# Kernel tuning notes

Measured on AMD Instinct MI355X. Metric: run time of the kernel, lower is better.

## Reference

```python
import jax, jax.numpy as jnp
import numpy as np

N_NODES = 50000


def gcn_conv(x, src, dst, W, b):
    # PyG GCNConv: h = D^-1/2 (A+I) D^-1/2 (x W) + b, aggregation at dst.
    n = x.shape[0]
    deg = jax.ops.segment_sum(jnp.ones_like(dst, dtype=x.dtype), dst, num_segments=n)
    dinv = jnp.where(deg > 0, jax.lax.rsqrt(deg), 0.0)
    norm = dinv[src] * dinv[dst]                      # [E]
    h = x @ W                                         # [N, out]
    msg = h[src] * norm[:, None]                      # [E, out] gather
    out = jax.ops.segment_sum(msg, dst, num_segments=n)  # scatter-add
    return out + b


def setup_inputs() -> dict:
    key = jax.random.key(0)
    k1, k2, k3, k4 = jax.random.split(key, 4)
    in_dim, hid, out_dim = 128, 256, 128
    x = jax.random.normal(k1, (N_NODES, in_dim), dtype=jnp.float32)
    edge_index = jax.random.randint(k2, (2, 800000), 0, N_NODES, dtype=jnp.int64)
    s1 = 1.0 / np.sqrt(in_dim)
    s2 = 1.0 / np.sqrt(hid)
    W1 = jax.random.uniform(k3, (in_dim, hid), jnp.float32, -s1, s1)
    b1 = jnp.zeros((hid,), jnp.float32)
    W2 = jax.random.uniform(k4, (hid, out_dim), jnp.float32, -s2, s2)
    b2 = jnp.zeros((out_dim,), jnp.float32)
    return {"x": x, "edge_index": edge_index, "W1": W1, "b1": b1, "W2": W2, "b2": b2}


def reference(x, edge_index, W1, b1, W2, b2):
    n = x.shape[0]
    loops = jnp.arange(n, dtype=edge_index.dtype)
    src = jnp.concatenate([edge_index[0], loops])  # add self-loops
    dst = jnp.concatenate([edge_index[1], loops])
    h = jax.nn.relu(gcn_conv(x, src, dst, W1, b1))
    # dropout in eval mode -> identity
    return gcn_conv(h, src, dst, W2, b2)
```

## Files before the change

### kernel.cpp

```cpp
#include <hip/hip_runtime.h>
#include <hip/hip_bf16.h>


typedef __bf16 bf16x8v __attribute__((ext_vector_type(8)));
typedef short  s16x8   __attribute__((ext_vector_type(8)));
typedef float  f32x4   __attribute__((ext_vector_type(4)));

#define IN_DIM 128
#define HID    256
#define OUTD   128
#define BKT_SHIFT 7
#define BKT_NODES 128
#define MAXB 512
#define CAP  8192
#define EBLK 512

__device__ __forceinline__ float2 bf2f(__hip_bfloat162 v) {
    return make_float2(__bfloat162float(v.x), __bfloat162float(v.y));
}
__device__ __forceinline__ __hip_bfloat162 f2bf(float a, float b) {
    __hip_bfloat162 r; r.x = __float2bfloat16(a); r.y = __float2bfloat16(b); return r;
}
__device__ __forceinline__ void acc_row(float* acc, s16x8 r) {
    __hip_bfloat162* p = (__hip_bfloat162*)&r;
#pragma unroll
    for (int j = 0; j < 4; ++j) {
        float2 f = bf2f(p[j]);
        acc[2 * j]     += f.x;
        acc[2 * j + 1] += f.y;
    }
}

__device__ __forceinline__ int detect_f32(const void* W2raw) {
    const unsigned short* u = (const unsigned short*)W2raw;
    int f32 = 0;
#pragma unroll
    for (int i = 0; i < 64; ++i) {
        unsigned e = (u[i] >> 7) & 0xFF;
        if (e >= 0x7F) f32 = 1;
    }
    return f32;
}
__device__ __forceinline__ int detect_i64(const void* eiraw) {
    const unsigned* ip = (const unsigned*)eiraw;
    unsigned orodd = 0;
#pragma unroll
    for (int i = 0; i < 64; ++i) orodd |= ip[2 * i + 1];
    return (orodd == 0) ? 1 : 0;
}

__device__ __forceinline__ short ldw(const void* raw, int idx, int f32) {
    if (f32) {
        __hip_bfloat16 h = __float2bfloat16(((const float*)raw)[idx]);
        return *(short*)&h;
    }
    return ((const short*)raw)[idx];
}

template <int K, int NN>
__device__ __forceinline__ void swz_one(const void* Wraw, int f32,
                                        short* __restrict__ Bsw, int tid) {
    constexpr int KC = K / 32;
    constexpr int NT = NN / 16;
    if (tid >= NT * KC * 64) return;
    int lane = tid & 63;
    int kc   = (tid >> 6) % KC;
    int nt   = tid / (64 * KC);
    int n  = nt * 16 + (lane & 15);
    int kb = kc * 32 + (lane >> 4) * 8;
    s16x8 v;
#pragma unroll
    for (int j = 0; j < 8; ++j) v[j] = ldw(Wraw, (kb + j) * NN + n, f32);
    ((s16x8*)Bsw)[tid] = v;
}


__global__ __launch_bounds__(256) void k_pe(
        const void* __restrict__ ei_, int E, int N, int NB,
        int* __restrict__ bcnt, unsigned* __restrict__ ppack,
        const void* W1raw, const void* b1raw, const void* W2raw, const void* b2raw,
        short* __restrict__ Bsw1, short* __restrict__ Bsw2,
        __hip_bfloat16* __restrict__ b1c, __hip_bfloat16* __restrict__ b2c,
        int* __restrict__ flags) {
    int blk = blockIdx.x, t = threadIdx.x;
    if (blk >= EBLK) {
        int f32 = detect_f32(W2raw);
        int pb = blk - EBLK;
        if (pb < 16) {
            swz_one<IN_DIM, HID>(W1raw, f32, Bsw1, pb * 256 + t);
        } else if (pb < 32) {
            swz_one<HID, OUTD>(W2raw, f32, Bsw2, (pb - 16) * 256 + t);
        } else {
            short s1 = ldw(b1raw, t, f32);
            b1c[t] = *(__hip_bfloat16*)&s1;
            if (t < OUTD) {
                short s2 = ldw(b2raw, t, f32);
                b2c[t] = *(__hip_bfloat16*)&s2;
            }
            if (t == 0) {
                flags[0] = f32;
                flags[1] = detect_i64(ei_);
            }
        }
        return;
    }
    __shared__ int lhist[4][MAXB];
    __shared__ int lbase[4][MAXB];
    int wv = t >> 6;
    int i64 = detect_i64(ei_);
    const long long* p64 = (const long long*)ei_;
    const int*       p32 = (const int*)ei_;
    int per = (E + EBLK - 1) / EBLK;
    int e0 = blk * per, e1 = min(e0 + per, E);
    for (int i = t; i < NB; i += 256) {
        lhist[0][i] = 0; lhist[1][i] = 0; lhist[2][i] = 0; lhist[3][i] = 0;
    }
    __syncthreads();
    for (int e = e0 + t; e < e1; e += 256) {
        int d = i64 ? (int)p64[E + e] : p32[E + e];
        if ((unsigned)d >= (unsigned)N) d = 0;
        atomicAdd(&lhist[wv][((unsigned)d) >> BKT_SHIFT], 1);
    }
    __syncthreads();
    for (int i = t; i < NB; i += 256) {
        int c0 = lhist[0][i], c1 = lhist[1][i], c2 = lhist[2][i], c3 = lhist[3][i];
        int tot = c0 + c1 + c2 + c3;
        int g = tot ? atomicAdd(&bcnt[i], tot) : 0;
        lbase[0][i] = g;
        lbase[1][i] = g + c0;
        lbase[2][i] = g + c0 + c1;
        lbase[3][i] = g + c0 + c1 + c2;
        lhist[0][i] = 0; lhist[1][i] = 0; lhist[2][i] = 0; lhist[3][i] = 0;
    }
    __syncthreads();
    for (int e = e0 + t; e < e1; e += 256) {
        int d = i64 ? (int)p64[E + e] : p32[E + e];
        int s = i64 ? (int)p64[e]     : p32[e];
        if ((unsigned)d >= (unsigned)N) d = 0;
        if ((unsigned)s >= (unsigned)N) s = 0;
        int b = ((unsigned)d) >> BKT_SHIFT;
        int pos = lbase[wv][b] + atomicAdd(&lhist[wv][b], 1);
        if (pos < CAP)
            ppack[(size_t)b * CAP + pos] = ((unsigned)(d & (BKT_NODES - 1)) << 25) | (unsigned)s;
    }
}


__global__ __launch_bounds__(512) void k_bsort(const int* __restrict__ bcnt,
                                               const unsigned* __restrict__ ppack,
                                               int NB,
                                               int* __restrict__ csr, int* __restrict__ offsets,
                                               float* __restrict__ dinv, int N,
                                               const void* __restrict__ xraw,
                                               const int* __restrict__ flags,
                                               __hip_bfloat16* __restrict__ xs) {
    __shared__ int sb[MAXB];
    __shared__ int h[BKT_NODES], base[BKT_NODES], s[BKT_NODES];
    __shared__ float sdv[BKT_NODES];
    int b = blockIdx.x;
    int t = threadIdx.x;
    int c = (t < NB) ? min(bcnt[t], CAP) : 0;
    sb[t] = c;
    __syncthreads();
    for (int off = 1; off < MAXB; off <<= 1) {
        int u = (t >= off) ? sb[t - off] : 0;
        __syncthreads();
        sb[t] += u;
        __syncthreads();
    }
    int cnt   = min(bcnt[b], CAP);
    int ebase = sb[b] - cnt;
    if (b == NB - 1 && t == 0) offsets[N] = sb[b];
    const unsigned* pp = ppack + (size_t)b * CAP;
    if (t < BKT_NODES) h[t] = 0;
    __syncthreads();
    for (int e = t; e < cnt; e += 512) atomicAdd(&h[pp[e] >> 25], 1);
    __syncthreads();
    int v = (t < BKT_NODES) ? h[t] : 0;
    if (t < BKT_NODES) s[t] = v;
    __syncthreads();
    for (int off = 1; off < BKT_NODES; off <<= 1) {
        int u = (t < BKT_NODES && t >= off) ? s[t - off] : 0;
        __syncthreads();
        if (t < BKT_NODES) s[t] += u;
        __syncthreads();
    }
    if (t < BKT_NODES) {
        int excl = s[t] - v;
        base[t] = excl;
        int node = b * BKT_NODES + t;
        float dv = 0.f;
        if (node < N) {
            dv = rsqrtf((float)(v + 1));
            offsets[node] = ebase + excl;
            dinv[node] = dv;
        } else {
            dinv[node] = 0.f;
        }
        sdv[t] = dv;
        h[t] = 0;
    }
    __syncthreads();
    for (int e = t; e < cnt; e += 512) {
        unsigned pk = pp[e];
        int ld = pk >> 25;
        int pos = ebase + base[ld] + atomicAdd(&h[ld], 1);
        csr[pos] = (int)(pk & 0x1FFFFFFu);
    }
    int f32 = flags[0];
    if (!f32) {
        const s16x8* xg = (const s16x8*)xraw;
        s16x8* xo = (s16x8*)xs;
        for (int u = t; u < BKT_NODES * 16; u += 512) {
            int row = u >> 4;
            int node = b * BKT_NODES + row;
            float dv = sdv[row];
            s16x8 val = {0, 0, 0, 0, 0, 0, 0, 0};
            if (node < N) {
                s16x8 xin = xg[(size_t)node * 16 + (u & 15)];
                __hip_bfloat162* xp = (__hip_bfloat162*)&xin;
                __hip_bfloat162* vp = (__hip_bfloat162*)&val;
#pragma unroll
                for (int j = 0; j < 4; ++j) {
                    float2 f = bf2f(xp[j]);
                    vp[j] = f2bf(dv * f.x, dv * f.y);
                }
            }
            xo[(size_t)node * 16 + (u & 15)] = val;
        }
    } else {
        const float4* xg = (const float4*)xraw;
        __hip_bfloat162* xo = (__hip_bfloat162*)xs;
        for (int u = t; u < BKT_NODES * 32; u += 512) {
            int row = u >> 5;
            int node = b * BKT_NODES + row;
            float dv = sdv[row];
            __hip_bfloat162 v0 = f2bf(0.f, 0.f), v1 = v0;
            if (node < N) {
                float4 xin = xg[(size_t)node * 32 + (u & 31)];
                v0 = f2bf(dv * xin.x, dv * xin.y);
                v1 = f2bf(dv * xin.z, dv * xin.w);
            }
            xo[(size_t)node * 64 + (u & 31) * 2]     = v0;
            xo[(size_t)node * 64 + (u & 31) * 2 + 1] = v1;
        }
    }
}


__global__ __launch_bounds__(256) void k_agg1(
        const s16x8* __restrict__ xs8, const int* __restrict__ offsets,
        const int* __restrict__ csr, const float* __restrict__ dinv,
        s16x8* __restrict__ a8, int N, int Npad, int nwaves) {
    int gw   = blockIdx.x * 4 + (threadIdx.x >> 6);
    int lane = threadIdx.x & 63;
    int g = lane >> 4, li = lane & 15;
    for (int v = gw; v < Npad; v += nwaves) {
        if (v >= N) {
            if (g == 0) { s16x8 z = {0,0,0,0,0,0,0,0}; a8[(size_t)v * 16 + li] = z; }
            continue;
        }
        float acc[8];
#pragma unroll
        for (int j = 0; j < 8; ++j) acc[j] = 0.f;
        int o0 = offsets[v], o1 = offsets[v + 1];
        if (g == 0) acc_row(acc, xs8[(size_t)v * 16 + li]);
        int e = o0 + g;
        for (; e + 12 < o1; e += 16) {
            int s0 = csr[e], s1 = csr[e + 4], s2 = csr[e + 8], s3 = csr[e + 12];
            s16x8 r0 = xs8[(size_t)s0 * 16 + li];
            s16x8 r1 = xs8[(size_t)s1 * 16 + li];
            s16x8 r2 = xs8[(size_t)s2 * 16 + li];
            s16x8 r3 = xs8[(size_t)s3 * 16 + li];
            acc_row(acc, r0); acc_row(acc, r1); acc_row(acc, r2); acc_row(acc, r3);
        }
        for (; e < o1; e += 4) acc_row(acc, xs8[(size_t)csr[e] * 16 + li]);
#pragma unroll
        for (int j = 0; j < 8; ++j) {
            acc[j] += __shfl_xor(acc[j], 16, 64);
            acc[j] += __shfl_xor(acc[j], 32, 64);
        }
        if (g == 0) {
            float dv = dinv[v];
            s16x8 outv;
            __hip_bfloat162* op = (__hip_bfloat162*)&outv;
#pragma unroll
            for (int j = 0; j < 4; ++j) op[j] = f2bf(dv * acc[2 * j], dv * acc[2 * j + 1]);
            a8[(size_t)v * 16 + li] = outv;
        }
    }
}


__global__ __launch_bounds__(256) void k_gemm12(
        const __hip_bfloat16* __restrict__ A, const __hip_bfloat16* __restrict__ Bsw1,
        const __hip_bfloat16* __restrict__ b1c, const __hip_bfloat16* __restrict__ Bsw2,
        const float* __restrict__ dinv, __hip_bfloat16* __restrict__ h2s) {
    __shared__ __align__(16) __hip_bfloat16 hl[64 * HID];
    int wave = threadIdx.x >> 6, lane = threadIdx.x & 63;
    int quad = lane >> 4, l16 = lane & 15;
    int mw = wave * 16;
    int gm = blockIdx.x * 64 + mw;

    bf16x8v a1f[4];
#pragma unroll
    for (int kc = 0; kc < 4; ++kc)
        a1f[kc] = *reinterpret_cast<const bf16x8v*>(
            A + (size_t)(gm + l16) * IN_DIM + kc * 32 + quad * 8);

    const bf16x8v* B1 = reinterpret_cast<const bf16x8v*>(Bsw1);
    for (int nt = 0; nt < HID / 16; ++nt) {
        f32x4 acc = {0.f, 0.f, 0.f, 0.f};
#pragma unroll
        for (int kc = 0; kc < 4; ++kc)
            acc = __builtin_amdgcn_mfma_f32_16x16x32_bf16(a1f[kc], B1[(nt * 4 + kc) * 64 + lane], acc, 0, 0, 0);
        int col = nt * 16 + l16;
        int gcol = col >> 3, csub = col & 7;
        float bv = __bfloat162float(b1c[col]);
#pragma unroll
        for (int r = 0; r < 4; ++r) {
            float v0 = acc[r] + bv; v0 = v0 > 0.f ? v0 : 0.f;
            int r0 = mw + quad * 4 + r;
            ((__hip_bfloat16*)((char*)hl + (size_t)r0 * (HID * 2) + ((gcol ^ (r0 & 31)) << 4)))[csub] = __float2bfloat16(v0);
        }
    }

    bf16x8v a2f[8];
#pragma unroll
    for (int kc = 0; kc < 8; ++kc) {
        int row = mw + l16;
        int g = (kc * 4 + quad) ^ (row & 31);
        a2f[kc] = *reinterpret_cast<const bf16x8v*>(
            (char*)hl + (size_t)row * (HID * 2) + ((size_t)g << 4));
    }
    const bf16x8v* B2 = reinterpret_cast<const bf16x8v*>(Bsw2);
    int rb0 = gm + quad * 4;
    float sc0[4];
#pragma unroll
    for (int r = 0; r < 4; ++r) sc0[r] = dinv[rb0 + r];
    for (int nt = 0; nt < OUTD / 16; ++nt) {
        f32x4 acc = {0.f, 0.f, 0.f, 0.f};
#pragma unroll
        for (int kc = 0; kc < 8; ++kc)
            acc = __builtin_amdgcn_mfma_f32_16x16x32_bf16(a2f[kc], B2[(nt * 8 + kc) * 64 + lane], acc, 0, 0, 0);
        int col = nt * 16 + l16;
#pragma unroll
        for (int r = 0; r < 4; ++r)
            h2s[(size_t)(rb0 + r) * OUTD + col] = __float2bfloat16(acc[r] * sc0[r]);
    }
}


__global__ __launch_bounds__(256) void k_agg2(
        const s16x8* __restrict__ h8, const int* __restrict__ offsets,
        const int* __restrict__ csr, const float* __restrict__ dinv,
        const __hip_bfloat16* __restrict__ b2c, const int* __restrict__ flags,
        void* __restrict__ outraw, int N, int nwaves) {
    int gw   = blockIdx.x * 4 + (threadIdx.x >> 6);
    int lane = threadIdx.x & 63;
    int g = lane >> 4, li = lane & 15;
    int f32 = flags[0];
    float bb[8];
    {
        s16x8 bv = ((const s16x8*)b2c)[li];
        __hip_bfloat162* bp = (__hip_bfloat162*)&bv;
#pragma unroll
        for (int j = 0; j < 4; ++j) {
            float2 f = bf2f(bp[j]);
            bb[2 * j] = f.x; bb[2 * j + 1] = f.y;
        }
    }
    for (int v = gw; v < N; v += nwaves) {
        float acc[8];
#pragma unroll
        for (int j = 0; j < 8; ++j) acc[j] = 0.f;
        int o0 = offsets[v], o1 = offsets[v + 1];
        if (g == 0) acc_row(acc, h8[(size_t)v * 16 + li]);
        int e = o0 + g;
        for (; e + 12 < o1; e += 16) {
            int s0 = csr[e], s1 = csr[e + 4], s2 = csr[e + 8], s3 = csr[e + 12];
            s16x8 r0 = h8[(size_t)s0 * 16 + li];
            s16x8 r1 = h8[(size_t)s1 * 16 + li];
            s16x8 r2 = h8[(size_t)s2 * 16 + li];
            s16x8 r3 = h8[(size_t)s3 * 16 + li];
            acc_row(acc, r0); acc_row(acc, r1); acc_row(acc, r2); acc_row(acc, r3);
        }
        for (; e < o1; e += 4) acc_row(acc, h8[(size_t)csr[e] * 16 + li]);
#pragma unroll
        for (int j = 0; j < 8; ++j) {
            acc[j] += __shfl_xor(acc[j], 16, 64);
            acc[j] += __shfl_xor(acc[j], 32, 64);
        }
        if (g == 0) {
            float dv = dinv[v];
            if (f32) {
                float4* of = (float4*)outraw;
                float4 o0v = {dv * acc[0] + bb[0], dv * acc[1] + bb[1],
                              dv * acc[2] + bb[2], dv * acc[3] + bb[3]};
                float4 o1v = {dv * acc[4] + bb[4], dv * acc[5] + bb[5],
                              dv * acc[6] + bb[6], dv * acc[7] + bb[7]};
                of[(size_t)v * 32 + li * 2]     = o0v;
                of[(size_t)v * 32 + li * 2 + 1] = o1v;
            } else {
                s16x8 outv;
                __hip_bfloat162* op = (__hip_bfloat162*)&outv;
#pragma unroll
                for (int j = 0; j < 4; ++j)
                    op[j] = f2bf(dv * acc[2 * j] + bb[2 * j], dv * acc[2 * j + 1] + bb[2 * j + 1]);
                ((s16x8*)outraw)[(size_t)v * 16 + li] = outv;
            }
        }
    }
}


extern "C" void kernel_launch(void* const* d_in, const int* in_sizes, int n_in,
                              void* d_out, int out_size, void* d_ws, size_t ws_size,
                              hipStream_t stream) {
    const void* x  = d_in[0];
    const void* ei = d_in[1];
    const void* W1 = d_in[2];
    const void* b1 = d_in[3];
    const void* W2 = d_in[4];
    const void* b2 = d_in[5];

    const int N = in_sizes[0] / IN_DIM;
    const int E = in_sizes[1] / 2;
    const int Npad = ((N + 127) / 128) * 128;
    const int NB = Npad / BKT_NODES;

    char* w = (char*)d_ws;
    auto alloc = [&](size_t bytes) -> void* {
        void* p = (void*)w;
        w += (bytes + 255) / 256 * 256;
        return p;
    };
    int*   flags   = (int*)alloc(256);
    int*   bcnt    = (int*)alloc((size_t)MAXB * 4);
    int*   offsets = (int*)alloc((size_t)(N + 1) * 4);
    float* dinv    = (float*)alloc((size_t)Npad * 4);
    unsigned* ppack = (unsigned*)alloc((size_t)NB * CAP * 4);
    int*   csr     = (int*)alloc((size_t)E * 4);
    short* Bsw1 = (short*)alloc((size_t)IN_DIM * HID * 2);
    short* Bsw2 = (short*)alloc((size_t)HID * OUTD * 2);
    __hip_bfloat16* b1c = (__hip_bfloat16*)alloc((size_t)HID * 2);
    __hip_bfloat16* b2c = (__hip_bfloat16*)alloc((size_t)OUTD * 2);
    __hip_bfloat16* xs  = (__hip_bfloat16*)alloc((size_t)Npad * IN_DIM * 2);
    __hip_bfloat16* a1  = (__hip_bfloat16*)alloc((size_t)Npad * IN_DIM * 2);
    __hip_bfloat16* h2s = xs;

    hipMemsetAsync(bcnt, 0, (size_t)MAXB * 4, stream);

    k_pe<<<EBLK + 33, 256, 0, stream>>>(ei, E, N, NB, bcnt, ppack,
                                        W1, b1, W2, b2, Bsw1, Bsw2, b1c, b2c, flags);

    k_bsort<<<NB, 512, 0, stream>>>(bcnt, ppack, NB, csr, offsets, dinv, N,
                                    x, flags, xs);

    const int aggBlocks = 3072, nwaves = aggBlocks * 4;
    k_agg1<<<aggBlocks, 256, 0, stream>>>((const s16x8*)xs, offsets, csr, dinv,
                                          (s16x8*)a1, N, Npad, nwaves);

    k_gemm12<<<Npad / 64, 256, 0, stream>>>(a1, (const __hip_bfloat16*)Bsw1, b1c,
                                            (const __hip_bfloat16*)Bsw2, dinv, h2s);

    k_agg2<<<aggBlocks, 256, 0, stream>>>((const s16x8*)h2s, offsets, csr, dinv,
                                          b2c, flags, d_out, N, nwaves);
}
```

Before: 213.5 us.

## Split feature columns into chunk-major layout to shrink gather working set

Feature matrices xs, a1 and h2s are stored chunk-major: four 32-column slabs, each contiguous over nodes. The aggregation kernels launch one grid section per slab, and each wave handles one node with 16 edge groups of 4 lanes. The intent is to cut the random-gather working set per slab (about 3.2 MB of bf16) so it stays cache-resident, at the cost of reading the CSR and offsets four times and using smaller 64-byte gathers. The GEMM load and store indexing is updated to the new layout.

Result: slower. 289.8 us (+35.7%).

```diff
diff --git a/kernel.cpp b/kernel.cpp
--- a/kernel.cpp
+++ b/kernel.cpp
@@ -14,6 +14,8 @@
 #define MAXB 512
 #define CAP  8192
 #define EBLK 512
+#define NCHUNK 4
+#define AGG_CBLK 2048
 
 __device__ __forceinline__ float2 bf2f(__hip_bfloat162 v) {
     return make_float2(__bfloat162float(v.x), __bfloat162float(v.y));
@@ -150,7 +152,7 @@
                                                const unsigned* __restrict__ ppack,
                                                int NB,
                                                int* __restrict__ csr, int* __restrict__ offsets,
-                                               float* __restrict__ dinv, int N,
+                                               float* __restrict__ dinv, int N, int Npad,
                                                const void* __restrict__ xraw,
                                                const int* __restrict__ flags,
                                                __hip_bfloat16* __restrict__ xs) {
@@ -213,11 +215,12 @@
         s16x8* xo = (s16x8*)xs;
         for (int u = t; u < BKT_NODES * 16; u += 512) {
             int row = u >> 4;
+            int sl  = u & 15;
             int node = b * BKT_NODES + row;
             float dv = sdv[row];
             s16x8 val = {0, 0, 0, 0, 0, 0, 0, 0};
             if (node < N) {
-                s16x8 xin = xg[(size_t)node * 16 + (u & 15)];
+                s16x8 xin = xg[(size_t)node * 16 + sl];
                 __hip_bfloat162* xp = (__hip_bfloat162*)&xin;
                 __hip_bfloat162* vp = (__hip_bfloat162*)&val;
 #pragma unroll
@@ -226,23 +229,25 @@
                     vp[j] = f2bf(dv * f.x, dv * f.y);
                 }
             }
-            xo[(size_t)node * 16 + (u & 15)] = val;
+            xo[((size_t)(sl >> 2) * Npad + node) * 4 + (sl & 3)] = val;
         }
     } else {
         const float4* xg = (const float4*)xraw;
         __hip_bfloat162* xo = (__hip_bfloat162*)xs;
         for (int u = t; u < BKT_NODES * 32; u += 512) {
             int row = u >> 5;
+            int q   = u & 31;
             int node = b * BKT_NODES + row;
             float dv = sdv[row];
             __hip_bfloat162 v0 = f2bf(0.f, 0.f), v1 = v0;
             if (node < N) {
-                float4 xin = xg[(size_t)node * 32 + (u & 31)];
+                float4 xin = xg[(size_t)node * 32 + q];
                 v0 = f2bf(dv * xin.x, dv * xin.y);
                 v1 = f2bf(dv * xin.z, dv * xin.w);
             }
-            xo[(size_t)node * 64 + (u & 31) * 2]     = v0;
-            xo[(size_t)node * 64 + (u & 31) * 2 + 1] = v1;
+            size_t bi = ((size_t)(q >> 3) * Npad + node) * 16 + (q & 7) * 2;
+            xo[bi]     = v0;
+            xo[bi + 1] = v1;
         }
     }
 }
@@ -252,31 +257,29 @@
         const s16x8* __restrict__ xs8, const int* __restrict__ offsets,
         const int* __restrict__ csr, const float* __restrict__ dinv,
         s16x8* __restrict__ a8, int N, int Npad, int nwaves) {
-    int gw   = blockIdx.x * 4 + (threadIdx.x >> 6);
+    int chunk = blockIdx.x / AGG_CBLK;
+    int cb    = blockIdx.x % AGG_CBLK;
+    int gw   = cb * 4 + (threadIdx.x >> 6);
     int lane = threadIdx.x & 63;
-    int g = lane >> 4, li = lane & 15;
+    int g = lane >> 2, li = lane & 3;
+    const s16x8* xc = xs8 + (size_t)chunk * Npad * 4;
+    s16x8*       ac = a8  + (size_t)chunk * Npad * 4;
     for (int v = gw; v < Npad; v += nwaves) {
         if (v >= N) {
-            if (g == 0) { s16x8 z = {0,0,0,0,0,0,0,0}; a8[(size_t)v * 16 + li] = z; }
+            if (g == 0) { s16x8 z = {0,0,0,0,0,0,0,0}; ac[(size_t)v * 4 + li] = z; }
             continue;
         }
         float acc[8];
 #pragma unroll
         for (int j = 0; j < 8; ++j) acc[j] = 0.f;
         int o0 = offsets[v], o1 = offsets[v + 1];
-        if (g == 0) acc_row(acc, xs8[(size_t)v * 16 + li]);
-        int e = o0 + g;
-        for (; e + 12 < o1; e += 16) {
-            int s0 = csr[e], s1 = csr[e + 4], s2 = csr[e + 8], s3 = csr[e + 12];
-            s16x8 r0 = xs8[(size_t)s0 * 16 + li];
-            s16x8 r1 = xs8[(size_t)s1 * 16 + li];
-            s16x8 r2 = xs8[(size_t)s2 * 16 + li];
-            s16x8 r3 = xs8[(size_t)s3 * 16 + li];
-            acc_row(acc, r0); acc_row(acc, r1); acc_row(acc, r2); acc_row(acc, r3);
-        }
-        for (; e < o1; e += 4) acc_row(acc, xs8[(size_t)csr[e] * 16 + li]);
+        if (g == 0) acc_row(acc, xc[(size_t)v * 4 + li]);
+        for (int e = o0 + g; e < o1; e += 16)
+            acc_row(acc, xc[(size_t)csr[e] * 4 + li]);
 #pragma unroll
         for (int j = 0; j < 8; ++j) {
+            acc[j] += __shfl_xor(acc[j], 4, 64);
+            acc[j] += __shfl_xor(acc[j], 8, 64);
             acc[j] += __shfl_xor(acc[j], 16, 64);
             acc[j] += __shfl_xor(acc[j], 32, 64);
         }
@@ -286,7 +289,7 @@
             __hip_bfloat162* op = (__hip_bfloat162*)&outv;
 #pragma unroll
             for (int j = 0; j < 4; ++j) op[j] = f2bf(dv * acc[2 * j], dv * acc[2 * j + 1]);
-            a8[(size_t)v * 16 + li] = outv;
+            ac[(size_t)v * 4 + li] = outv;
         }
     }
 }
@@ -295,7 +298,7 @@
 __global__ __launch_bounds__(256) void k_gemm12(
         const __hip_bfloat16* __restrict__ A, const __hip_bfloat16* __restrict__ Bsw1,
         const __hip_bfloat16* __restrict__ b1c, const __hip_bfloat16* __restrict__ Bsw2,
-        const float* __restrict__ dinv, __hip_bfloat16* __restrict__ h2s) {
+        const float* __restrict__ dinv, __hip_bfloat16* __restrict__ h2s, int Npad) {
     __shared__ __align__(16) __hip_bfloat16 hl[64 * HID];
     int wave = threadIdx.x >> 6, lane = threadIdx.x & 63;
     int quad = lane >> 4, l16 = lane & 15;
@@ -306,7 +309,7 @@
 #pragma unroll
     for (int kc = 0; kc < 4; ++kc)
         a1f[kc] = *reinterpret_cast<const bf16x8v*>(
-            A + (size_t)(gm + l16) * IN_DIM + kc * 32 + quad * 8);
+            A + ((size_t)kc * Npad + gm + l16) * 32 + quad * 8);
 
     const bf16x8v* B1 = reinterpret_cast<const bf16x8v*>(Bsw1);
     for (int nt = 0; nt < HID / 16; ++nt) {
@@ -346,7 +349,7 @@
         int col = nt * 16 + l16;
 #pragma unroll
         for (int r = 0; r < 4; ++r)
-            h2s[(size_t)(rb0 + r) * OUTD + col] = __float2bfloat16(acc[r] * sc0[r]);
+            h2s[((size_t)(nt >> 1) * Npad + rb0 + r) * 32 + (col & 31)] = __float2bfloat16(acc[r] * sc0[r]);
     }
 }
 
@@ -355,14 +358,17 @@
         const s16x8* __restrict__ h8, const int* __restrict__ offsets,
         const int* __restrict__ csr, const float* __restrict__ dinv,
         const __hip_bfloat16* __restrict__ b2c, const int* __restrict__ flags,
-        void* __restrict__ outraw, int N, int nwaves) {
-    int gw   = blockIdx.x * 4 + (threadIdx.x >> 6);
+        void* __restrict__ outraw, int N, int Npad, int nwaves) {
+    int chunk = blockIdx.x / AGG_CBLK;
+    int cb    = blockIdx.x % AGG_CBLK;
+    int gw   = cb * 4 + (threadIdx.x >> 6);
     int lane = threadIdx.x & 63;
-    int g = lane >> 4, li = lane & 15;
+    int g = lane >> 2, li = lane & 3;
     int f32 = flags[0];
+    const s16x8* hc = h8 + (size_t)chunk * Npad * 4;
     float bb[8];
     {
-        s16x8 bv = ((const s16x8*)b2c)[li];
+        s16x8 bv = ((const s16x8*)b2c)[chunk * 4 + li];
         __hip_bfloat162* bp = (__hip_bfloat162*)&bv;
 #pragma unroll
         for (int j = 0; j < 4; ++j) {
@@ -375,19 +381,13 @@
 #pragma unroll
         for (int j = 0; j < 8; ++j) acc[j] = 0.f;
         int o0 = offsets[v], o1 = offsets[v + 1];
-        if (g == 0) acc_row(acc, h8[(size_t)v * 16 + li]);
-        int e = o0 + g;
-        for (; e + 12 < o1; e += 16) {
-            int s0 = csr[e], s1 = csr[e + 4], s2 = csr[e + 8], s3 = csr[e + 12];
-            s16x8 r0 = h8[(size_t)s0 * 16 + li];
-            s16x8 r1 = h8[(size_t)s1 * 16 + li];
-            s16x8 r2 = h8[(size_t)s2 * 16 + li];
-            s16x8 r3 = h8[(size_t)s3 * 16 + li];
-            acc_row(acc, r0); acc_row(acc, r1); acc_row(acc, r2); acc_row(acc, r3);
-        }
-        for (; e < o1; e += 4) acc_row(acc, h8[(size_t)csr[e] * 16 + li]);
+        if (g == 0) acc_row(acc, hc[(size_t)v * 4 + li]);
+        for (int e = o0 + g; e < o1; e += 16)
+            acc_row(acc, hc[(size_t)csr[e] * 4 + li]);
 #pragma unroll
         for (int j = 0; j < 8; ++j) {
+            acc[j] += __shfl_xor(acc[j], 4, 64);
+            acc[j] += __shfl_xor(acc[j], 8, 64);
             acc[j] += __shfl_xor(acc[j], 16, 64);
             acc[j] += __shfl_xor(acc[j], 32, 64);
         }
@@ -399,15 +399,15 @@
                               dv * acc[2] + bb[2], dv * acc[3] + bb[3]};
                 float4 o1v = {dv * acc[4] + bb[4], dv * acc[5] + bb[5],
                               dv * acc[6] + bb[6], dv * acc[7] + bb[7]};
-                of[(size_t)v * 32 + li * 2]     = o0v;
-                of[(size_t)v * 32 + li * 2 + 1] = o1v;
+                of[(size_t)v * 32 + chunk * 8 + li * 2]     = o0v;
+                of[(size_t)v * 32 + chunk * 8 + li * 2 + 1] = o1v;
             } else {
                 s16x8 outv;
                 __hip_bfloat162* op = (__hip_bfloat162*)&outv;
 #pragma unroll
                 for (int j = 0; j < 4; ++j)
                     op[j] = f2bf(dv * acc[2 * j] + bb[2 * j], dv * acc[2 * j + 1] + bb[2 * j + 1]);
-                ((s16x8*)outraw)[(size_t)v * 16 + li] = outv;
+                ((s16x8*)outraw)[(size_t)v * 16 + chunk * 4 + li] = outv;
             }
         }
     }
@@ -454,16 +454,16 @@
     k_pe<<<EBLK + 33, 256, 0, stream>>>(ei, E, N, NB, bcnt, ppack,
                                         W1, b1, W2, b2, Bsw1, Bsw2, b1c, b2c, flags);
 
-    k_bsort<<<NB, 512, 0, stream>>>(bcnt, ppack, NB, csr, offsets, dinv, N,
+    k_bsort<<<NB, 512, 0, stream>>>(bcnt, ppack, NB, csr, offsets, dinv, N, Npad,
                                     x, flags, xs);
 
-    const int aggBlocks = 3072, nwaves = aggBlocks * 4;
+    const int aggBlocks = NCHUNK * AGG_CBLK, nwaves = AGG_CBLK * 4;
     k_agg1<<<aggBlocks, 256, 0, stream>>>((const s16x8*)xs, offsets, csr, dinv,
                                           (s16x8*)a1, N, Npad, nwaves);
 
     k_gemm12<<<Npad / 64, 256, 0, stream>>>(a1, (const __hip_bfloat16*)Bsw1, b1c,
-                                            (const __hip_bfloat16*)Bsw2, dinv, h2s);
+                                            (const __hip_bfloat16*)Bsw2, dinv, h2s, Npad);
 
     k_agg2<<<aggBlocks, 256, 0, stream>>>((const s16x8*)h2s, offsets, csr, dinv,
-                                          b2c, flags, d_out, N, nwaves);
-}
+                                          b2c, flags, d_out, N, Npad, nwaves);
+}
```

## Map one node per quarter-wave in aggregation kernels instead of splitting edges

Applied to the files above, without the earlier changes.

Both aggregation kernels now assign each node to a 16-lane quarter-wave and launch one thread slot per node, replacing the grid-stride loop where a whole wave split a node's edges four ways. This removes the cross-quarter shuffle reduction and the idle lanes on the final store. It also uses 32-bit byte-offset addressing and nontemporal loads and stores for the CSR indices and outputs. The cost is that the four nodes sharing a wave can have different degrees, so quarters diverge and lanes sit idle.

Measured after the change: 211.6 us. About the same (-0.9%).

```diff
diff --git a/kernel.cpp b/kernel.cpp
--- a/kernel.cpp
+++ b/kernel.cpp
@@ -251,44 +251,46 @@
 __global__ __launch_bounds__(256) void k_agg1(
         const s16x8* __restrict__ xs8, const int* __restrict__ offsets,
         const int* __restrict__ csr, const float* __restrict__ dinv,
-        s16x8* __restrict__ a8, int N, int Npad, int nwaves) {
+        s16x8* __restrict__ a8, int N, int Npad) {
     int gw   = blockIdx.x * 4 + (threadIdx.x >> 6);
     int lane = threadIdx.x & 63;
-    int g = lane >> 4, li = lane & 15;
-    for (int v = gw; v < Npad; v += nwaves) {
-        if (v >= N) {
-            if (g == 0) { s16x8 z = {0,0,0,0,0,0,0,0}; a8[(size_t)v * 16 + li] = z; }
-            continue;
-        }
-        float acc[8];
-#pragma unroll
-        for (int j = 0; j < 8; ++j) acc[j] = 0.f;
-        int o0 = offsets[v], o1 = offsets[v + 1];
-        if (g == 0) acc_row(acc, xs8[(size_t)v * 16 + li]);
-        int e = o0 + g;
-        for (; e + 12 < o1; e += 16) {
-            int s0 = csr[e], s1 = csr[e + 4], s2 = csr[e + 8], s3 = csr[e + 12];
-            s16x8 r0 = xs8[(size_t)s0 * 16 + li];
-            s16x8 r1 = xs8[(size_t)s1 * 16 + li];
-            s16x8 r2 = xs8[(size_t)s2 * 16 + li];
-            s16x8 r3 = xs8[(size_t)s3 * 16 + li];
-            acc_row(acc, r0); acc_row(acc, r1); acc_row(acc, r2); acc_row(acc, r3);
-        }
-        for (; e < o1; e += 4) acc_row(acc, xs8[(size_t)csr[e] * 16 + li]);
-#pragma unroll
-        for (int j = 0; j < 8; ++j) {
-            acc[j] += __shfl_xor(acc[j], 16, 64);
-            acc[j] += __shfl_xor(acc[j], 32, 64);
-        }
-        if (g == 0) {
-            float dv = dinv[v];
-            s16x8 outv;
-            __hip_bfloat162* op = (__hip_bfloat162*)&outv;
-#pragma unroll
-            for (int j = 0; j < 4; ++j) op[j] = f2bf(dv * acc[2 * j], dv * acc[2 * j + 1]);
-            a8[(size_t)v * 16 + li] = outv;
-        }
-    }
+    int quad = lane >> 4, l16 = lane & 15;
+    int v = gw * 4 + quad;
+    if (v >= Npad) return;
+    const char* xb = (const char*)xs8;
+    unsigned go = ((unsigned)v << 8) | ((unsigned)l16 << 4);
+    if (v >= N) {
+        s16x8 z = {0, 0, 0, 0, 0, 0, 0, 0};
+        *(s16x8*)((char*)a8 + go) = z;
+        return;
+    }
+    float acc[8];
+#pragma unroll
+    for (int j = 0; j < 8; ++j) acc[j] = 0.f;
+    int o0 = offsets[v], o1 = offsets[v + 1];
+    acc_row(acc, *(const s16x8*)(xb + go));
+    int e = o0;
+    for (; e + 3 < o1; e += 4) {
+        int s0 = __builtin_nontemporal_load(&csr[e]);
+        int s1 = __builtin_nontemporal_load(&csr[e + 1]);
+        int s2 = __builtin_nontemporal_load(&csr[e + 2]);
+        int s3 = __builtin_nontemporal_load(&csr[e + 3]);
+        s16x8 r0 = *(const s16x8*)(xb + (((unsigned)s0 << 8) | ((unsigned)l16 << 4)));
+        s16x8 r1 = *(const s16x8*)(xb + (((unsigned)s1 << 8) | ((unsigned)l16 << 4)));
+        s16x8 r2 = *(const s16x8*)(xb + (((unsigned)s2 << 8) | ((unsigned)l16 << 4)));
+        s16x8 r3 = *(const s16x8*)(xb + (((unsigned)s3 << 8) | ((unsigned)l16 << 4)));
+        acc_row(acc, r0); acc_row(acc, r1); acc_row(acc, r2); acc_row(acc, r3);
+    }
+    for (; e < o1; ++e) {
+        int s0 = __builtin_nontemporal_load(&csr[e]);
+        acc_row(acc, *(const s16x8*)(xb + (((unsigned)s0 << 8) | ((unsigned)l16 << 4))));
+    }
+    float dv = dinv[v];
+    s16x8 outv;
+    __hip_bfloat162* op = (__hip_bfloat162*)&outv;
+#pragma unroll
+    for (int j = 0; j < 4; ++j) op[j] = f2bf(dv * acc[2 * j], dv * acc[2 * j + 1]);
+    *(s16x8*)((char*)a8 + go) = outv;
 }
 
 
@@ -355,14 +357,15 @@
         const s16x8* __restrict__ h8, const int* __restrict__ offsets,
         const int* __restrict__ csr, const float* __restrict__ dinv,
         const __hip_bfloat16* __restrict__ b2c, const int* __restrict__ flags,
-        void* __restrict__ outraw, int N, int nwaves) {
+        void* __restrict__ outraw, int N) {
     int gw   = blockIdx.x * 4 + (threadIdx.x >> 6);
     int lane = threadIdx.x & 63;
-    int g = lane >> 4, li = lane & 15;
+    int quad = lane >> 4, l16 = lane & 15;
     int f32 = flags[0];
+    const char* hb = (const char*)h8;
     float bb[8];
     {
-        s16x8 bv = ((const s16x8*)b2c)[li];
+        s16x8 bv = ((const s16x8*)b2c)[l16];
         __hip_bfloat162* bp = (__hip_bfloat162*)&bv;
 #pragma unroll
         for (int j = 0; j < 4; ++j) {
@@ -370,46 +373,45 @@
             bb[2 * j] = f.x; bb[2 * j + 1] = f.y;
         }
     }
-    for (int v = gw; v < N; v += nwaves) {
-        float acc[8];
-#pragma unroll
-        for (int j = 0; j < 8; ++j) acc[j] = 0.f;
-        int o0 = offsets[v], o1 = offsets[v + 1];
-        if (g == 0) acc_row(acc, h8[(size_t)v * 16 + li]);
-        int e = o0 + g;
-        for (; e + 12 < o1; e += 16) {
-            int s0 = csr[e], s1 = csr[e + 4], s2 = csr[e + 8], s3 = csr[e + 12];
-            s16x8 r0 = h8[(size_t)s0 * 16 + li];
-            s16x8 r1 = h8[(size_t)s1 * 16 + li];
-            s16x8 r2 = h8[(size_t)s2 * 16 + li];
-            s16x8 r3 = h8[(size_t)s3 * 16 + li];
-            acc_row(acc, r0); acc_row(acc, r1); acc_row(acc, r2); acc_row(acc, r3);
-        }
-        for (; e < o1; e += 4) acc_row(acc, h8[(size_t)csr[e] * 16 + li]);
-#pragma unroll
-        for (int j = 0; j < 8; ++j) {
-            acc[j] += __shfl_xor(acc[j], 16, 64);
-            acc[j] += __shfl_xor(acc[j], 32, 64);
-        }
-        if (g == 0) {
-            float dv = dinv[v];
-            if (f32) {
-                float4* of = (float4*)outraw;
-                float4 o0v = {dv * acc[0] + bb[0], dv * acc[1] + bb[1],
-                              dv * acc[2] + bb[2], dv * acc[3] + bb[3]};
-                float4 o1v = {dv * acc[4] + bb[4], dv * acc[5] + bb[5],
-                              dv * acc[6] + bb[6], dv * acc[7] + bb[7]};
-                of[(size_t)v * 32 + li * 2]     = o0v;
-                of[(size_t)v * 32 + li * 2 + 1] = o1v;
-            } else {
-                s16x8 outv;
-                __hip_bfloat162* op = (__hip_bfloat162*)&outv;
-#pragma unroll
-                for (int j = 0; j < 4; ++j)
-                    op[j] = f2bf(dv * acc[2 * j] + bb[2 * j], dv * acc[2 * j + 1] + bb[2 * j + 1]);
-                ((s16x8*)outraw)[(size_t)v * 16 + li] = outv;
-            }
-        }
+    int v = gw * 4 + quad;
+    if (v >= N) return;
+    float acc[8];
+#pragma unroll
+    for (int j = 0; j < 8; ++j) acc[j] = 0.f;
+    int o0 = offsets[v], o1 = offsets[v + 1];
+    acc_row(acc, *(const s16x8*)(hb + (((unsigned)v << 8) | ((unsigned)l16 << 4))));
+    int e = o0;
+    for (; e + 3 < o1; e += 4) {
+        int s0 = __builtin_nontemporal_load(&csr[e]);
+        int s1 = __builtin_nontemporal_load(&csr[e + 1]);
+        int s2 = __builtin_nontemporal_load(&csr[e + 2]);
+        int s3 = __builtin_nontemporal_load(&csr[e + 3]);
+        s16x8 r0 = *(const s16x8*)(hb + (((unsigned)s0 << 8) | ((unsigned)l16 << 4)));
+        s16x8 r1 = *(const s16x8*)(hb + (((unsigned)s1 << 8) | ((unsigned)l16 << 4)));
+        s16x8 r2 = *(const s16x8*)(hb + (((unsigned)s2 << 8) | ((unsigned)l16 << 4)));
+        s16x8 r3 = *(const s16x8*)(hb + (((unsigned)s3 << 8) | ((unsigned)l16 << 4)));
+        acc_row(acc, r0); acc_row(acc, r1); acc_row(acc, r2); acc_row(acc, r3);
+    }
+    for (; e < o1; ++e) {
+        int s0 = __builtin_nontemporal_load(&csr[e]);
+        acc_row(acc, *(const s16x8*)(hb + (((unsigned)s0 << 8) | ((unsigned)l16 << 4))));
+    }
+    float dv = dinv[v];
+    if (f32) {
+        f32x4* of = (f32x4*)outraw;
+        f32x4 o0v = {dv * acc[0] + bb[0], dv * acc[1] + bb[1],
+                     dv * acc[2] + bb[2], dv * acc[3] + bb[3]};
+        f32x4 o1v = {dv * acc[4] + bb[4], dv * acc[5] + bb[5],
+                     dv * acc[6] + bb[6], dv * acc[7] + bb[7]};
+        __builtin_nontemporal_store(o0v, &of[(size_t)v * 32 + l16 * 2]);
+        __builtin_nontemporal_store(o1v, &of[(size_t)v * 32 + l16 * 2 + 1]);
+    } else {
+        s16x8 outv;
+        __hip_bfloat162* op = (__hip_bfloat162*)&outv;
+#pragma unroll
+        for (int j = 0; j < 4; ++j)
+            op[j] = f2bf(dv * acc[2 * j] + bb[2 * j], dv * acc[2 * j + 1] + bb[2 * j + 1]);
+        __builtin_nontemporal_store(outv, &((s16x8*)outraw)[(size_t)v * 16 + l16]);
     }
 }
 
@@ -457,13 +459,13 @@
     k_bsort<<<NB, 512, 0, stream>>>(bcnt, ppack, NB, csr, offsets, dinv, N,
                                     x, flags, xs);
 
-    const int aggBlocks = 3072, nwaves = aggBlocks * 4;
-    k_agg1<<<aggBlocks, 256, 0, stream>>>((const s16x8*)xs, offsets, csr, dinv,
-                                          (s16x8*)a1, N, Npad, nwaves);
+    k_agg1<<<Npad / 16, 256, 0, stream>>>((const s16x8*)xs, offsets, csr, dinv,
+                                          (s16x8*)a1, N, Npad);
 
     k_gemm12<<<Npad / 64, 256, 0, stream>>>(a1, (const __hip_bfloat16*)Bsw1, b1c,
                                             (const __hip_bfloat16*)Bsw2, dinv, h2s);
 
-    k_agg2<<<aggBlocks, 256, 0, stream>>>((const s16x8*)h2s, offsets, csr, dinv,
-                                          b2c, flags, d_out, N, nwaves);
-}
+    const int agg2Blocks = (N + 15) / 16;
+    k_agg2<<<agg2Blocks, 256, 0, stream>>>((const s16x8*)h2s, offsets, csr, dinv,
+                                           b2c, flags, d_out, N);
+}
```
